# Performance work log

Measured on AMD Instinct MI355X. Metric: run time of the kernel, lower is better.

Reference implementation:

```python
import jax, jax.numpy as jnp
import numpy as np

HIDDEN = 128
B, N, S = 4, 200, 512  # batch, 200 segments, 512 tokens each (hard-coded in source view())


def setup_inputs() -> dict:
    key = jax.random.key(0)
    ks = jax.random.split(key, 7)
    query = jax.random.normal(ks[0], (B, HIDDEN), dtype=jnp.float32)
    context = jax.random.normal(ks[1], (B, N, S, HIDDEN), dtype=jnp.float32)
    context_mask = jax.random.uniform(ks[2], (B, N, S), dtype=jnp.float32)
    scale = 1.0 / np.sqrt(HIDDEN)
    Wq = jax.random.normal(ks[3], (HIDDEN, HIDDEN), dtype=jnp.float32) * scale
    bq = jax.random.normal(ks[4], (HIDDEN,), dtype=jnp.float32) * 0.01
    Wc = jax.random.normal(ks[5], (HIDDEN, HIDDEN), dtype=jnp.float32) * scale
    bc = jax.random.normal(ks[6], (HIDDEN,), dtype=jnp.float32) * 0.01
    return {"query": query, "context": context, "context_mask": context_mask,
            "Wq": Wq, "bq": bq, "Wc": Wc, "bc": bc}


def reference(query, context, context_mask, Wq, bq, Wc, bc):
    # q_projection / c_projection (nn.Linear: x @ W.T + b)
    q = query @ Wq.T + bq                      # [B, H]
    c = context @ Wc.T + bc                    # [B, N, S, H]
    # bmm(reshape_c, q) -> scores [B, N, S]
    att = jnp.einsum('bnsh,bh->bns', c, q)
    masked_att = att * context_mask            # multiplicative mask (as in source)
    w = jax.nn.softmax(masked_att, axis=-1)    # [B, N, S]
    # fused dual-axis weighted reductions (avoid [B,N,S,H] broadcast materialization)
    result = jnp.einsum('bns,bnsh->bnh', w, context)       # sum over tokens S
    token_result = jnp.einsum('bns,bnsh->bsh', w, context)  # sum over segments N
    return (result, token_result)
```

## Files before the change

### kernel.cpp

```cpp
#include <hip/hip_runtime.h>
#include <hip/hip_bf16.h>
#include <math.h>

#define H    128
#define NB   4
#define NSEG 200
#define NS   512


__global__ void precompute_kernel(const float* __restrict__ query,
                                  const float* __restrict__ Wq,
                                  const float* __restrict__ bq,
                                  const float* __restrict__ Wc,
                                  const float* __restrict__ bc,
                                  float* __restrict__ v_out,
                                  float* __restrict__ c0_out) {
    __shared__ float qsh[H];
    __shared__ float red[H];
    const int tid = threadIdx.x;
    for (int b = 0; b < NB; ++b) {
        float acc = bq[tid];
        const float* qr = query + b * H;
        const float* wr = Wq + tid * H;
        for (int k = 0; k < H; ++k) acc += qr[k] * wr[k];
        qsh[tid] = acc;
        __syncthreads();
        float vacc = 0.f;
        for (int h2 = 0; h2 < H; ++h2) vacc += qsh[h2] * Wc[h2 * H + tid];
        v_out[b * H + tid] = vacc;
        red[tid] = qsh[tid] * bc[tid];
        __syncthreads();
        for (int off = H / 2; off > 0; off >>= 1) {
            if (tid < off) red[tid] += red[tid + off];
            __syncthreads();
        }
        if (tid == 0) c0_out[b] = red[0];
        __syncthreads();
    }
}

__global__ __launch_bounds__(512)
void att_softmax_result_kernel(const float* __restrict__ context,
                               const float* __restrict__ mask,
                               const float* __restrict__ v,
                               const float* __restrict__ c0,
                               float* __restrict__ w_out,
                               float* __restrict__ result_out) {
    __shared__ float  vv[H];
    __shared__ float  sc[NS];
    __shared__ float  red[NS];
    __shared__ float4 red4[16 * 32];

    const int tid = threadIdx.x;
    const int blk = blockIdx.x;
    const int b   = blk / NSEG;
    const float* ctx = context + (size_t)blk * NS * H;

    if (tid < H) vv[tid] = v[b * H + tid];
    const float c0b = c0[b];
    __syncthreads();

    {
        const int s = tid;
        const float4* crow = (const float4*)(ctx + (size_t)s * H);
        float acc = c0b;
        #pragma unroll
        for (int k = 0; k < H / 4; ++k) {
            float4 cv = crow[k];
            acc += cv.x * vv[4 * k + 0] + cv.y * vv[4 * k + 1]
                 + cv.z * vv[4 * k + 2] + cv.w * vv[4 * k + 3];
        }
        acc *= mask[(size_t)blk * NS + s];
        sc[s]  = acc;
        red[s] = acc;
    }
    __syncthreads();

    for (int off = NS / 2; off > 0; off >>= 1) {
        if (tid < off) red[tid] = fmaxf(red[tid], red[tid + off]);
        __syncthreads();
    }
    const float mx = red[0];
    __syncthreads();
    const float e = __expf(sc[tid] - mx);
    sc[tid]  = e;
    red[tid] = e;
    __syncthreads();
    for (int off = NS / 2; off > 0; off >>= 1) {
        if (tid < off) red[tid] += red[tid + off];
        __syncthreads();
    }
    const float inv = 1.0f / red[0];
    const float wv  = e * inv;
    sc[tid] = wv;
    w_out[(size_t)blk * NS + tid] = wv;
    __syncthreads();

    {
        const int h4 = tid & 31;
        const int g  = tid >> 5;
        float4 acc = {0.f, 0.f, 0.f, 0.f};
        const float4* c4 = (const float4*)ctx;
        for (int s = g; s < NS; s += 16) {
            const float ws_ = sc[s];
            float4 cv = c4[(size_t)s * 32 + h4];
            acc.x += ws_ * cv.x; acc.y += ws_ * cv.y;
            acc.z += ws_ * cv.z; acc.w += ws_ * cv.w;
        }
        red4[g * 32 + h4] = acc;
        __syncthreads();
        for (int off = 8; off > 0; off >>= 1) {
            if (g < off) {
                float4 o = red4[(g + off) * 32 + h4];
                float4 m = red4[g * 32 + h4];
                m.x += o.x; m.y += o.y; m.z += o.z; m.w += o.w;
                red4[g * 32 + h4] = m;
            }
            __syncthreads();
        }
        if (g == 0)
            ((float4*)result_out)[(size_t)blk * 32 + h4] = red4[h4];
    }
}

__global__ __launch_bounds__(256)
void token_partial_kernel(const float* __restrict__ context,
                          const float* __restrict__ w,
                          float* __restrict__ out,
                          int nsplit) {
    const int tiles = NB * NS / 8;
    const int tile  = blockIdx.x % tiles;
    const int split = blockIdx.x / tiles;
    const int n_per = NSEG / nsplit;
    const int n0 = split * n_per, n1 = n0 + n_per;

    const int tid = threadIdx.x;
    const int h4  = tid & 31;
    const int j   = tid >> 5;
    const int b   = tile / (NS / 8);
    const int s   = (tile % (NS / 8)) * 8 + j;

    float4 acc = {0.f, 0.f, 0.f, 0.f};
    #pragma unroll 4
    for (int n = n0; n < n1; ++n) {
        const size_t row = (size_t)(b * NSEG + n) * NS + s;
        const float wv = w[row];
        float4 cv = ((const float4*)context)[row * 32 + h4];
        acc.x += wv * cv.x; acc.y += wv * cv.y;
        acc.z += wv * cv.z; acc.w += wv * cv.w;
    }
    ((float4*)out)[(size_t)split * (NB * NS * H / 4)
                   + ((size_t)b * NS + s) * 32 + h4] = acc;
}

__global__ void combine_kernel(const float* __restrict__ part,
                               float* __restrict__ out, int nsplit) {
    const int i = blockIdx.x * blockDim.x + threadIdx.x;
    const float4* p = (const float4*)part;
    float4 acc = p[i];
    for (int sp = 1; sp < nsplit; ++sp) {
        float4 o = p[(size_t)sp * (NB * NS * H / 4) + i];
        acc.x += o.x; acc.y += o.y; acc.z += o.z; acc.w += o.w;
    }
    ((float4*)out)[i] = acc;
}

extern "C" void kernel_launch(void* const* d_in, const int* in_sizes, int n_in,
                              void* d_out, int out_size, void* d_ws, size_t ws_size,
                              hipStream_t stream) {
    const float* query   = (const float*)d_in[0];
    const float* context = (const float*)d_in[1];
    const float* mask    = (const float*)d_in[2];
    const float* Wq      = (const float*)d_in[3];
    const float* bq      = (const float*)d_in[4];
    const float* Wc      = (const float*)d_in[5];
    const float* bc      = (const float*)d_in[6];

    float* out = (float*)d_out;
    float* wsf = (float*)d_ws;

    float* v    = wsf;
    float* c0   = wsf + 512;
    float* w    = wsf + 1024;
    float* part = wsf + 1024 + NB * NSEG * NS;

    float* result_out = out;
    float* token_out  = out + NB * NSEG * H;

    const size_t need_split = (size_t)(1024 + NB * NSEG * NS + 4 * NB * NS * H) * sizeof(float);
    const int nsplit = (ws_size >= need_split) ? 4 : 1;

    precompute_kernel<<<1, 128, 0, stream>>>(query, Wq, bq, Wc, bc, v, c0);
    att_softmax_result_kernel<<<NB * NSEG, 512, 0, stream>>>(
        context, mask, v, c0, w, result_out);
    if (nsplit == 4) {
        token_partial_kernel<<<4 * NB * NS / 8, 256, 0, stream>>>(context, w, part, 4);
        combine_kernel<<<NB * NS * H / 4 / 256, 256, 0, stream>>>(part, token_out, 4);
    } else {
        token_partial_kernel<<<NB * NS / 8, 256, 0, stream>>>(context, w, token_out, 1);
    }
}
```

Before: 391.8 us.

## Split scores/softmax and fuse segment and token weighted sums into tiled kernel

Splits the scores/softmax pass into its own kernel. Each warp now reads one context row in a coalesced way and reduces it with lane shuffles, with warp-shuffle max/sum for the softmax. The segment sum and the token sum are computed together by one tiled kernel over (10 segments x 64 tokens) tiles, so the second context pass feeds both reductions. Partial results go to workspace and are summed by two small combine kernels. The precompute kernel is also spread across one block per batch. This adds about 24 MB of partial-sum traffic and assumes the workspace is large enough, without the old size check.

New measurement: 353.8 us. 1.11x faster.

```diff
diff --git a/kernel.cpp b/kernel.cpp
--- a/kernel.cpp
+++ b/kernel.cpp
@@ -6,6 +6,10 @@
 #define NB   4
 #define NSEG 200
 #define NS   512
+#define GN   10
+#define GS   64
+#define NGRP (NSEG / GN)
+#define NST  (NS / GS)
 
 
 __global__ void precompute_kernel(const float* __restrict__ query,
@@ -18,148 +22,195 @@
     __shared__ float qsh[H];
     __shared__ float red[H];
     const int tid = threadIdx.x;
-    for (int b = 0; b < NB; ++b) {
-        float acc = bq[tid];
-        const float* qr = query + b * H;
-        const float* wr = Wq + tid * H;
-        for (int k = 0; k < H; ++k) acc += qr[k] * wr[k];
-        qsh[tid] = acc;
+    const int b   = blockIdx.x;
+    float acc = bq[tid];
+    const float* qr = query + b * H;
+    const float* wr = Wq + tid * H;
+    for (int k = 0; k < H; ++k) acc += qr[k] * wr[k];
+    qsh[tid] = acc;
+    __syncthreads();
+    float vacc = 0.f;
+    for (int h2 = 0; h2 < H; ++h2) vacc += qsh[h2] * Wc[h2 * H + tid];
+    v_out[b * H + tid] = vacc;
+    red[tid] = qsh[tid] * bc[tid];
+    __syncthreads();
+    for (int off = H / 2; off > 0; off >>= 1) {
+        if (tid < off) red[tid] += red[tid + off];
         __syncthreads();
-        float vacc = 0.f;
-        for (int h2 = 0; h2 < H; ++h2) vacc += qsh[h2] * Wc[h2 * H + tid];
-        v_out[b * H + tid] = vacc;
-        red[tid] = qsh[tid] * bc[tid];
-        __syncthreads();
-        for (int off = H / 2; off > 0; off >>= 1) {
-            if (tid < off) red[tid] += red[tid + off];
-            __syncthreads();
-        }
-        if (tid == 0) c0_out[b] = red[0];
-        __syncthreads();
-    }
+    }
+    if (tid == 0) c0_out[b] = red[0];
 }
 
 __global__ __launch_bounds__(512)
-void att_softmax_result_kernel(const float* __restrict__ context,
-                               const float* __restrict__ mask,
-                               const float* __restrict__ v,
-                               const float* __restrict__ c0,
-                               float* __restrict__ w_out,
-                               float* __restrict__ result_out) {
-    __shared__ float  vv[H];
+void scores_softmax_kernel(const float* __restrict__ context,
+                           const float* __restrict__ mask,
+                           const float* __restrict__ v,
+                           const float* __restrict__ c0,
+                           float* __restrict__ w_out) {
+    __shared__ float4 vv4[32];
+    __shared__ float  mk[NS];
     __shared__ float  sc[NS];
-    __shared__ float  red[NS];
-    __shared__ float4 red4[16 * 32];
+    __shared__ float  wred[8];
 
     const int tid = threadIdx.x;
     const int blk = blockIdx.x;
     const int b   = blk / NSEG;
-    const float* ctx = context + (size_t)blk * NS * H;
-
-    if (tid < H) vv[tid] = v[b * H + tid];
+    const float* cseg = context + (size_t)blk * NS * H;
+
+    if (tid < 32) vv4[tid] = ((const float4*)(v + b * H))[tid];
+    mk[tid] = mask[(size_t)blk * NS + tid];
+    __syncthreads();
+
+    const int   h4  = tid & 31;
+    const int   rg  = tid >> 5;
     const float c0b = c0[b];
-    __syncthreads();
-
-    {
-        const int s = tid;
-        const float4* crow = (const float4*)(ctx + (size_t)s * H);
-        float acc = c0b;
+
+    #pragma unroll 4
+    for (int it = 0; it < NS / 16; ++it) {
+        const int s = it * 16 + rg;
+        const float4 cv = ((const float4*)(cseg + (size_t)s * H))[h4];
+        const float4 vq = vv4[h4];
+        float p = cv.x * vq.x + cv.y * vq.y + cv.z * vq.z + cv.w * vq.w;
+        p += __shfl_xor(p, 16);
+        p += __shfl_xor(p, 8);
+        p += __shfl_xor(p, 4);
+        p += __shfl_xor(p, 2);
+        p += __shfl_xor(p, 1);
+        if (h4 == 0) sc[s] = (p + c0b) * mk[s];
+    }
+    __syncthreads();
+
+    const float x = sc[tid];
+    float m = x;
+    for (int o = 32; o > 0; o >>= 1) m = fmaxf(m, __shfl_xor(m, o));
+    const int wid = tid >> 6, lane = tid & 63;
+    if (lane == 0) wred[wid] = m;
+    __syncthreads();
+    if (tid == 0) {
+        float mm = wred[0];
+        for (int i = 1; i < 8; ++i) mm = fmaxf(mm, wred[i]);
+        wred[0] = mm;
+    }
+    __syncthreads();
+    const float mx = wred[0];
+    const float e  = __expf(x - mx);
+    float ssum = e;
+    for (int o = 32; o > 0; o >>= 1) ssum += __shfl_xor(ssum, o);
+    __syncthreads();
+    if (lane == 0) wred[wid] = ssum;
+    __syncthreads();
+    if (tid == 0) {
+        float t = 0.f;
+        for (int i = 0; i < 8; ++i) t += wred[i];
+        wred[0] = t;
+    }
+    __syncthreads();
+    w_out[(size_t)blk * NS + tid] = e / wred[0];
+}
+
+__global__ __launch_bounds__(512)
+void weighted_kernel(const float* __restrict__ context,
+                     const float* __restrict__ w,
+                     float* __restrict__ result_part,
+                     float* __restrict__ token_part) {
+    const int bid = blockIdx.x;
+    const int st  = bid & (NST - 1);
+    const int tmp = bid / NST;
+    const int ng  = tmp % NGRP;
+    const int b   = tmp / NGRP;
+    const int n0  = ng * GN;
+    const int s0  = st * GS;
+
+    const int tid = threadIdx.x;
+    const int h4  = tid & 31;
+    const int rg  = tid >> 5;
+
+    __shared__ float  wt[GN * GS];
+    __shared__ float4 red4[5 * 16 * 32];
+
+    for (int i = tid; i < GN * GS; i += 512) {
+        const int nn = i >> 6, ss = i & (GS - 1);
+        wt[i] = w[((size_t)(b * NSEG + n0 + nn)) * NS + s0 + ss];
+    }
+    __syncthreads();
+
+    float4 racc[GN];
+    float4 tacc[4];
+    #pragma unroll
+    for (int n = 0; n < GN; ++n) racc[n] = make_float4(0.f, 0.f, 0.f, 0.f);
+    #pragma unroll
+    for (int j = 0; j < 4; ++j) tacc[j] = make_float4(0.f, 0.f, 0.f, 0.f);
+
+    #pragma unroll
+    for (int n = 0; n < GN; ++n) {
+        const float* base = context + ((size_t)(b * NSEG + n0 + n) * NS + s0) * (size_t)H;
         #pragma unroll
-        for (int k = 0; k < H / 4; ++k) {
-            float4 cv = crow[k];
-            acc += cv.x * vv[4 * k + 0] + cv.y * vv[4 * k + 1]
-                 + cv.z * vv[4 * k + 2] + cv.w * vv[4 * k + 3];
+        for (int j = 0; j < 4; ++j) {
+            const int s = j * 16 + rg;
+            const float  wv = wt[n * GS + s];
+            const float4 cv = ((const float4*)(base + (size_t)s * H))[h4];
+            racc[n].x += wv * cv.x; racc[n].y += wv * cv.y;
+            racc[n].z += wv * cv.z; racc[n].w += wv * cv.w;
+            tacc[j].x += wv * cv.x; tacc[j].y += wv * cv.y;
+            tacc[j].z += wv * cv.z; tacc[j].w += wv * cv.w;
         }
-        acc *= mask[(size_t)blk * NS + s];
-        sc[s]  = acc;
-        red[s] = acc;
-    }
-    __syncthreads();
-
-    for (int off = NS / 2; off > 0; off >>= 1) {
-        if (tid < off) red[tid] = fmaxf(red[tid], red[tid + off]);
-        __syncthreads();
-    }
-    const float mx = red[0];
-    __syncthreads();
-    const float e = __expf(sc[tid] - mx);
-    sc[tid]  = e;
-    red[tid] = e;
-    __syncthreads();
-    for (int off = NS / 2; off > 0; off >>= 1) {
-        if (tid < off) red[tid] += red[tid + off];
-        __syncthreads();
-    }
-    const float inv = 1.0f / red[0];
-    const float wv  = e * inv;
-    sc[tid] = wv;
-    w_out[(size_t)blk * NS + tid] = wv;
-    __syncthreads();
-
-    {
-        const int h4 = tid & 31;
-        const int g  = tid >> 5;
-        float4 acc = {0.f, 0.f, 0.f, 0.f};
-        const float4* c4 = (const float4*)ctx;
-        for (int s = g; s < NS; s += 16) {
-            const float ws_ = sc[s];
-            float4 cv = c4[(size_t)s * 32 + h4];
-            acc.x += ws_ * cv.x; acc.y += ws_ * cv.y;
-            acc.z += ws_ * cv.z; acc.w += ws_ * cv.w;
-        }
-        red4[g * 32 + h4] = acc;
+    }
+
+    #pragma unroll
+    for (int j = 0; j < 4; ++j) {
+        const int s = j * 16 + rg;
+        ((float4*)token_part)[(((size_t)ng * NB + b) * NS + s0 + s) * 32 + h4] = tacc[j];
+    }
+
+    for (int nb = 0; nb < GN; nb += 5) {
+        #pragma unroll
+        for (int j = 0; j < 5; ++j)
+            red4[(j * 16 + rg) * 32 + h4] = racc[nb + j];
         __syncthreads();
         for (int off = 8; off > 0; off >>= 1) {
-            if (g < off) {
-                float4 o = red4[(g + off) * 32 + h4];
-                float4 m = red4[g * 32 + h4];
-                m.x += o.x; m.y += o.y; m.z += o.z; m.w += o.w;
-                red4[g * 32 + h4] = m;
+            if (rg < off) {
+                #pragma unroll
+                for (int j = 0; j < 5; ++j) {
+                    float4 o = red4[(j * 16 + rg + off) * 32 + h4];
+                    float4 mm = red4[(j * 16 + rg) * 32 + h4];
+                    mm.x += o.x; mm.y += o.y; mm.z += o.z; mm.w += o.w;
+                    red4[(j * 16 + rg) * 32 + h4] = mm;
+                }
             }
             __syncthreads();
         }
-        if (g == 0)
-            ((float4*)result_out)[(size_t)blk * 32 + h4] = red4[h4];
-    }
-}
-
-__global__ __launch_bounds__(256)
-void token_partial_kernel(const float* __restrict__ context,
-                          const float* __restrict__ w,
-                          float* __restrict__ out,
-                          int nsplit) {
-    const int tiles = NB * NS / 8;
-    const int tile  = blockIdx.x % tiles;
-    const int split = blockIdx.x / tiles;
-    const int n_per = NSEG / nsplit;
-    const int n0 = split * n_per, n1 = n0 + n_per;
-
-    const int tid = threadIdx.x;
-    const int h4  = tid & 31;
-    const int j   = tid >> 5;
-    const int b   = tile / (NS / 8);
-    const int s   = (tile % (NS / 8)) * 8 + j;
-
+        if (rg == 0) {
+            #pragma unroll
+            for (int j = 0; j < 5; ++j)
+                ((float4*)result_part)[(((size_t)(b * NSEG + n0 + nb + j)) * NST + st) * 32 + h4]
+                    = red4[(j * 16) * 32 + h4];
+        }
+        __syncthreads();
+    }
+}
+
+__global__ void combine_result_kernel(const float* __restrict__ part,
+                                      float* __restrict__ out) {
+    const int i = blockIdx.x * blockDim.x + threadIdx.x;
+    const int row = i >> 5, h4 = i & 31;
     float4 acc = {0.f, 0.f, 0.f, 0.f};
-    #pragma unroll 4
-    for (int n = n0; n < n1; ++n) {
-        const size_t row = (size_t)(b * NSEG + n) * NS + s;
-        const float wv = w[row];
-        float4 cv = ((const float4*)context)[row * 32 + h4];
-        acc.x += wv * cv.x; acc.y += wv * cv.y;
-        acc.z += wv * cv.z; acc.w += wv * cv.w;
-    }
-    ((float4*)out)[(size_t)split * (NB * NS * H / 4)
-                   + ((size_t)b * NS + s) * 32 + h4] = acc;
-}
-
-__global__ void combine_kernel(const float* __restrict__ part,
-                               float* __restrict__ out, int nsplit) {
+    const float4* p = (const float4*)part;
+    #pragma unroll
+    for (int st = 0; st < NST; ++st) {
+        float4 o = p[((size_t)row * NST + st) * 32 + h4];
+        acc.x += o.x; acc.y += o.y; acc.z += o.z; acc.w += o.w;
+    }
+    ((float4*)out)[i] = acc;
+}
+
+__global__ void combine_token_kernel(const float* __restrict__ part,
+                                     float* __restrict__ out) {
     const int i = blockIdx.x * blockDim.x + threadIdx.x;
+    float4 acc = {0.f, 0.f, 0.f, 0.f};
     const float4* p = (const float4*)part;
-    float4 acc = p[i];
-    for (int sp = 1; sp < nsplit; ++sp) {
-        float4 o = p[(size_t)sp * (NB * NS * H / 4) + i];
+    #pragma unroll
+    for (int g = 0; g < NGRP; ++g) {
+        float4 o = p[(size_t)g * (NB * NS * H / 4) + i];
         acc.x += o.x; acc.y += o.y; acc.z += o.z; acc.w += o.w;
     }
     ((float4*)out)[i] = acc;
@@ -179,24 +230,18 @@
     float* out = (float*)d_out;
     float* wsf = (float*)d_ws;
 
-    float* v    = wsf;
-    float* c0   = wsf + 512;
-    float* w    = wsf + 1024;
-    float* part = wsf + 1024 + NB * NSEG * NS;
+    float* v     = wsf;
+    float* c0    = wsf + 512;
+    float* w     = wsf + 1024;
+    float* rpart = wsf + 1024 + NB * NSEG * NS;
+    float* tpart = rpart + NB * NSEG * NST * H;
 
     float* result_out = out;
     float* token_out  = out + NB * NSEG * H;
 
-    const size_t need_split = (size_t)(1024 + NB * NSEG * NS + 4 * NB * NS * H) * sizeof(float);
-    const int nsplit = (ws_size >= need_split) ? 4 : 1;
-
-    precompute_kernel<<<1, 128, 0, stream>>>(query, Wq, bq, Wc, bc, v, c0);
-    att_softmax_result_kernel<<<NB * NSEG, 512, 0, stream>>>(
-        context, mask, v, c0, w, result_out);
-    if (nsplit == 4) {
-        token_partial_kernel<<<4 * NB * NS / 8, 256, 0, stream>>>(context, w, part, 4);
-        combine_kernel<<<NB * NS * H / 4 / 256, 256, 0, stream>>>(part, token_out, 4);
-    } else {
-        token_partial_kernel<<<NB * NS / 8, 256, 0, stream>>>(context, w, token_out, 1);
-    }
-}
+    precompute_kernel<<<NB, 128, 0, stream>>>(query, Wq, bq, Wc, bc, v, c0);
+    scores_softmax_kernel<<<NB * NSEG, 512, 0, stream>>>(context, mask, v, c0, w);
+    weighted_kernel<<<NB * NGRP * NST, 512, 0, stream>>>(context, w, rpart, tpart);
+    combine_result_kernel<<<NB * NSEG * H / 4 / 256, 256, 0, stream>>>(rpart, result_out);
+    combine_token_kernel<<<NB * NS * H / 4 / 256, 256, 0, stream>>>(tpart, token_out);
+}
```
